# Kernel tuning notes

Hardware: AMD Instinct MI355X
Metric: run time of the kernel (lower is better)

The kernel has to match this reference:

```python
import jax, jax.numpy as jnp
import numpy as np

B, S, E, H = 4, 2048, 512, 8
DH = E // H
EPS = 1e-5

def _ln(x, g, b):
    m = jnp.mean(x, axis=-1, keepdims=True)
    v = jnp.var(x, axis=-1, keepdims=True)
    return (x - m) * jax.lax.rsqrt(v + EPS) * g + b

def setup_inputs() -> dict:
    key = jax.random.key(0)
    ks = jax.random.split(key, 8)
    sc = 0.02
    return {
        "x": jax.random.normal(ks[0], (B, S, E), dtype=jnp.float32),
        "ln1_g": jnp.ones((E,), jnp.float32),
        "ln1_b": jnp.zeros((E,), jnp.float32),
        "in_proj_w": sc * jax.random.normal(ks[1], (3 * E, E), jnp.float32),
        "in_proj_b": jnp.zeros((3 * E,), jnp.float32),
        "out_w": sc * jax.random.normal(ks[2], (E, E), jnp.float32),
        "out_b": jnp.zeros((E,), jnp.float32),
        "ln2_g": jnp.ones((E,), jnp.float32),
        "ln2_b": jnp.zeros((E,), jnp.float32),
        "fc1_w": sc * jax.random.normal(ks[3], (E, E), jnp.float32),
        "fc1_b": jnp.zeros((E,), jnp.float32),
        "fc2_w": sc * jax.random.normal(ks[4], (E, E), jnp.float32),
        "fc2_b": jnp.zeros((E,), jnp.float32),
    }

def reference(x, ln1_g, ln1_b, in_proj_w, in_proj_b, out_w, out_b,
              ln2_g, ln2_b, fc1_w, fc1_b, fc2_w, fc2_b):
    # pre-LN
    z = _ln(x, ln1_g, ln1_b)
    # qkv projection (torch MHA packed in_proj: [3E, E])
    qkv = z @ in_proj_w.T + in_proj_b          # [B,S,3E]
    q, k, v = jnp.split(qkv, 3, axis=-1)
    q = q.reshape(B, S, H, DH)
    k = k.reshape(B, S, H, DH)
    v = v.reshape(B, S, H, DH)
    scores = jnp.einsum("bqhd,bkhd->bhqk", q, k) / np.sqrt(DH).astype(np.float32)
    causal = jnp.triu(jnp.ones((S, S), dtype=bool), k=1)  # True = masked
    neg = jnp.finfo(scores.dtype).min
    scores = jnp.where(causal, neg, scores)
    attn = jax.nn.softmax(scores, axis=-1)      # [B,H,S,S]
    ctx = jnp.einsum("bhqk,bkhd->bqhd", attn, v).reshape(B, S, E)
    attn_out = ctx @ out_w.T + out_b
    # torch MHA with need_weights=True averages over heads by default
    attn_weights = jnp.mean(attn, axis=1)       # [B,S,S]
    z2 = x + attn_out
    y = _ln(z2, ln2_g, ln2_b)
    y = jax.nn.leaky_relu(y @ fc1_w.T + fc1_b, negative_slope=0.01)
    y = y @ fc2_w.T + fc2_b
    y = y + z2
    return (y, attn_weights)
```

## Files before the change

### kernel.cpp

```cpp
#include <hip/hip_runtime.h>

typedef short bf16x8 __attribute__((ext_vector_type(8)));
typedef float f32x4 __attribute__((ext_vector_type(4)));
typedef unsigned short u16x8 __attribute__((ext_vector_type(8)));

#define NB 4
#define SQ 2048
#define EM 512
#define NH 8
#define DHD 64
#define QSCALE 0.1803368801111731f

__device__ __forceinline__ unsigned short f2bf(float x) {
  unsigned u = __float_as_uint(x);
  u += 0x7FFFu + ((u >> 16) & 1u);
  return (unsigned short)(u >> 16);
}

__device__ __forceinline__ int sw8(int row, int col8) { return col8 ^ ((row & 7) << 3); }

__device__ __forceinline__ void glds16(const void* g, void* l) {
  __builtin_amdgcn_global_load_lds(
      (const __attribute__((address_space(1))) void*)g,
      (__attribute__((address_space(3))) void*)l, 16, 0, 0);
}

__global__ __launch_bounds__(256) void f2bf4_kernel(
    const float* __restrict__ w0, const float* __restrict__ w1,
    const float* __restrict__ w2, const float* __restrict__ w3,
    unsigned short* __restrict__ o0, unsigned short* __restrict__ o1,
    unsigned short* __restrict__ o2, unsigned short* __restrict__ o3) {
  int i = (blockIdx.x * 256 + threadIdx.x) * 8;
  const float* src;
  unsigned short* dst;
  int off;
  if (i < 786432) { src = w0; dst = o0; off = i; }
  else if (i < 1048576) { src = w1; dst = o1; off = i - 786432; }
  else if (i < 1310720) { src = w2; dst = o2; off = i - 1048576; }
  else { src = w3; dst = o3; off = i - 1310720; }
  f32x4 a = *(const f32x4*)(src + off);
  f32x4 b = *(const f32x4*)(src + off + 4);
  u16x8 o;
#pragma unroll
  for (int j = 0; j < 4; ++j) { o[j] = f2bf(a[j]); o[j + 4] = f2bf(b[j]); }
  *(u16x8*)(dst + off) = o;
}

__global__ __launch_bounds__(256) void ln_kernel(const float* __restrict__ x,
                                                 const float* __restrict__ g,
                                                 const float* __restrict__ bb,
                                                 unsigned short* __restrict__ out) {
  int tid = threadIdx.x;
  int row = blockIdx.x * 4 + (tid >> 6);
  int lane = tid & 63;
  size_t base = (size_t)row * EM + lane * 8;
  f32x4 v0 = *(const f32x4*)(x + base);
  f32x4 v1 = *(const f32x4*)(x + base + 4);
  float s = 0.f, q = 0.f;
#pragma unroll
  for (int j = 0; j < 4; ++j) { s += v0[j] + v1[j]; q += v0[j] * v0[j] + v1[j] * v1[j]; }
#pragma unroll
  for (int m = 1; m < 64; m <<= 1) { s += __shfl_xor(s, m); q += __shfl_xor(q, m); }
  float mean = s * (1.f / EM);
  float var = q * (1.f / EM) - mean * mean;
  float rs = rsqrtf(var + 1e-5f);
  f32x4 g0 = *(const f32x4*)(g + lane * 8), g1 = *(const f32x4*)(g + lane * 8 + 4);
  f32x4 b0 = *(const f32x4*)(bb + lane * 8), b1 = *(const f32x4*)(bb + lane * 8 + 4);
  u16x8 o;
#pragma unroll
  for (int j = 0; j < 4; ++j) {
    o[j] = f2bf((v0[j] - mean) * rs * g0[j] + b0[j]);
    o[j + 4] = f2bf((v1[j] - mean) * rs * g1[j] + b1[j]);
  }
  *(u16x8*)(out + base) = o;
}

template <bool LEAKY, bool RESID, bool OUTF32, bool QKV>
__global__ __launch_bounds__(256) void gemm64(
    const unsigned short* __restrict__ A, const unsigned short* __restrict__ Bm,
    const float* __restrict__ bias, const float* __restrict__ resid,
    float* __restrict__ outf, unsigned short* __restrict__ outh,
    unsigned short* __restrict__ qo, unsigned short* __restrict__ ko,
    unsigned short* __restrict__ vo, int M, int N, int K) {
  __shared__ unsigned short As[2][64][64];
  __shared__ unsigned short Bs[2][64][64];
  int m0 = blockIdx.x * 64, n0 = blockIdx.y * 64;
  int t = threadIdx.x;
  int wv = t >> 6, ln = t & 63, lg = ln >> 4, lr = ln & 15;
  int rsub = ln >> 3;
  int csw = ((ln & 7) ^ rsub) * 8;
  f32x4 acc[4];
#pragma unroll
  for (int c = 0; c < 4; ++c)
#pragma unroll
    for (int r = 0; r < 4; ++r) acc[c][r] = 0.f;

  const unsigned short* ag0 = A + (size_t)(m0 + wv * 16 + rsub) * K + csw;
  const unsigned short* ag1 = A + (size_t)(m0 + wv * 16 + 8 + rsub) * K + csw;
  const unsigned short* bg0 = Bm + (size_t)(n0 + wv * 16 + rsub) * K + csw;
  const unsigned short* bg1 = Bm + (size_t)(n0 + wv * 16 + 8 + rsub) * K + csw;

  glds16(ag0, &As[0][wv * 16][0]);
  glds16(ag1, &As[0][wv * 16 + 8][0]);
  glds16(bg0, &Bs[0][wv * 16][0]);
  glds16(bg1, &Bs[0][wv * 16 + 8][0]);

  int nk = K >> 6;
  for (int ki = 0; ki < nk; ++ki) {
    int cur = ki & 1;
    __syncthreads();
    if (ki + 1 < nk) {
      int nb = cur ^ 1;
      int ko_ = (ki + 1) * 64;
      glds16(ag0 + ko_, &As[nb][wv * 16][0]);
      glds16(ag1 + ko_, &As[nb][wv * 16 + 8][0]);
      glds16(bg0 + ko_, &Bs[nb][wv * 16][0]);
      glds16(bg1 + ko_, &Bs[nb][wv * 16 + 8][0]);
    }
#pragma unroll
    for (int kk = 0; kk < 64; kk += 32) {
      int arw = wv * 16 + lr;
      bf16x8 af = *(const bf16x8*)&As[cur][arw][sw8(arw, kk + lg * 8)];
#pragma unroll
      for (int c = 0; c < 4; ++c) {
        int brw = c * 16 + lr;
        bf16x8 bf = *(const bf16x8*)&Bs[cur][brw][sw8(brw, kk + lg * 8)];
        acc[c] = __builtin_amdgcn_mfma_f32_16x16x32_bf16(af, bf, acc[c], 0, 0, 0);
      }
    }
  }
#pragma unroll
  for (int c = 0; c < 4; ++c) {
    int C_ = n0 + c * 16 + lr;
    float bv = bias[C_];
#pragma unroll
    for (int r = 0; r < 4; ++r) {
      int R_ = m0 + wv * 16 + lg * 4 + r;
      float v = acc[c][r] + bv;
      if (LEAKY) v = v > 0.f ? v : 0.01f * v;
      if (RESID) v += resid[(size_t)R_ * N + C_];
      if (QKV) {
        int which = C_ >> 9, f = C_ & 511, h = f >> 6, d = f & 63;
        int b_ = R_ >> 11, s_ = R_ & 2047;
        if (which == 0) {
          qo[(((size_t)b_ * NH + h) * SQ + s_) * DHD + d] = f2bf(v * QSCALE);
        } else if (which == 1) {
          ko[(((size_t)b_ * NH + h) * SQ + s_) * DHD + d] = f2bf(v);
        } else {
          vo[(((size_t)b_ * NH + h) * DHD + d) * SQ + s_] = f2bf(v);
        }
      } else if (OUTF32) {
        outf[(size_t)R_ * N + C_] = v;
      } else {
        outh[(size_t)R_ * N + C_] = f2bf(v);
      }
    }
  }
}

template <bool QKV>
__global__ __launch_bounds__(256) void gemm128(
    const unsigned short* __restrict__ A, const unsigned short* __restrict__ Bm,
    const float* __restrict__ bias, unsigned short* __restrict__ qo,
    unsigned short* __restrict__ ko, unsigned short* __restrict__ vo,
    int M, int N, int K) {
  __shared__ unsigned short As[2][128][64];
  __shared__ unsigned short Bs[2][128][64];
  int m0 = blockIdx.x * 128, n0 = blockIdx.y * 128;
  int t = threadIdx.x;
  int wv = t >> 6, ln = t & 63, lg = ln >> 4, lr = ln & 15;
  int wr = wv >> 1, wc = wv & 1;
  int rsub = ln >> 3;
  int csw = ((ln & 7) ^ rsub) * 8;
  f32x4 acc[4][4];
#pragma unroll
  for (int m = 0; m < 4; ++m)
#pragma unroll
    for (int n = 0; n < 4; ++n)
#pragma unroll
      for (int r = 0; r < 4; ++r) acc[m][n][r] = 0.f;

  const unsigned short* agb = A + (size_t)(m0 + wv * 8 + rsub) * K + csw;
  const unsigned short* bgb = Bm + (size_t)(n0 + wv * 8 + rsub) * K + csw;

#pragma unroll
  for (int i = 0; i < 4; ++i) {
    glds16(agb + (size_t)(i * 32) * K, &As[0][i * 32 + wv * 8][0]);
    glds16(bgb + (size_t)(i * 32) * K, &Bs[0][i * 32 + wv * 8][0]);
  }

  int nk = K >> 6;
  for (int ki = 0; ki < nk; ++ki) {
    int cur = ki & 1;
    __syncthreads();
    if (ki + 1 < nk) {
      int nb = cur ^ 1;
      int ko_ = (ki + 1) * 64;
#pragma unroll
      for (int i = 0; i < 4; ++i) {
        glds16(agb + (size_t)(i * 32) * K + ko_, &As[nb][i * 32 + wv * 8][0]);
        glds16(bgb + (size_t)(i * 32) * K + ko_, &Bs[nb][i * 32 + wv * 8][0]);
      }
    }
#pragma unroll
    for (int kk = 0; kk < 64; kk += 32) {
      bf16x8 af[4], bfr[4];
#pragma unroll
      for (int m = 0; m < 4; ++m) {
        int arw = wr * 64 + m * 16 + lr;
        af[m] = *(const bf16x8*)&As[cur][arw][sw8(arw, kk + lg * 8)];
      }
#pragma unroll
      for (int n = 0; n < 4; ++n) {
        int brw = wc * 64 + n * 16 + lr;
        bfr[n] = *(const bf16x8*)&Bs[cur][brw][sw8(brw, kk + lg * 8)];
      }
#pragma unroll
      for (int m = 0; m < 4; ++m)
#pragma unroll
        for (int n = 0; n < 4; ++n)
          acc[m][n] = __builtin_amdgcn_mfma_f32_16x16x32_bf16(af[m], bfr[n], acc[m][n], 0, 0, 0);
    }
  }

#pragma unroll
  for (int n = 0; n < 4; ++n) {
    int C_ = n0 + wc * 64 + n * 16 + lr;
    float bv = bias[C_];
#pragma unroll
    for (int m = 0; m < 4; ++m) {
#pragma unroll
      for (int r = 0; r < 4; ++r) {
        int R_ = m0 + wr * 64 + m * 16 + lg * 4 + r;
        float v = acc[m][n][r] + bv;
        int which = C_ >> 9, f = C_ & 511, h = f >> 6, d = f & 63;
        int b_ = R_ >> 11, s_ = R_ & 2047;
        if (which == 0) {
          qo[(((size_t)b_ * NH + h) * SQ + s_) * DHD + d] = f2bf(v * QSCALE);
        } else if (which == 1) {
          ko[(((size_t)b_ * NH + h) * SQ + s_) * DHD + d] = f2bf(v);
        } else {
          vo[(((size_t)b_ * NH + h) * DHD + d) * SQ + s_] = f2bf(v);
        }
      }
    }
  }
}

__global__ __launch_bounds__(256) void flash_kernel(
    const unsigned short* __restrict__ Q, const unsigned short* __restrict__ Kb,
    const unsigned short* __restrict__ Vt, unsigned short* __restrict__ ctx,
    float* __restrict__ mstat, float* __restrict__ lstat) {
  __shared__ unsigned short Ks[2][64][64];
  __shared__ unsigned short Vs[2][64][64];
  __shared__ unsigned short Ps[4][16][64];
  int h = blockIdx.y, b = blockIdx.z;
  int t = threadIdx.x, wv = t >> 6, ln = t & 63, lg = ln >> 4, lr = ln & 15;
  int rsub = ln >> 3;
  int csw = ((ln & 7) ^ rsub) * 8;
  size_t headoff = ((size_t)b * NH + h) * SQ;
  const unsigned short* kg0 = Kb + (headoff + wv * 16 + rsub) * DHD + csw;
  const unsigned short* kg1 = Kb + (headoff + wv * 16 + 8 + rsub) * DHD + csw;
  const unsigned short* vg0 = Vt + (((size_t)b * NH + h) * DHD + wv * 16 + rsub) * SQ + csw;
  const unsigned short* vg1 = Vt + (((size_t)b * NH + h) * DHD + wv * 16 + 8 + rsub) * SQ + csw;

  bf16x8 vones;
#pragma unroll
  for (int j = 0; j < 8; ++j) vones[j] = (lr == 0) ? (short)0x3F80 : (short)0;

  for (int half = 0; half < 2; ++half) {
    int qt = half ? blockIdx.x : (31 - blockIdx.x);
    int qb = qt * 64;
    const unsigned short* qrow = Q + (headoff + qb + wv * 16 + lr) * DHD;
    bf16x8 aq0 = *(const bf16x8*)(qrow + lg * 8);
    bf16x8 aq1 = *(const bf16x8*)(qrow + 32 + lg * 8);

    f32x4 cacc[4], lacc;
#pragma unroll
    for (int nd = 0; nd < 4; ++nd)
#pragma unroll
      for (int r = 0; r < 4; ++r) cacc[nd][r] = 0.f;
#pragma unroll
    for (int r = 0; r < 4; ++r) lacc[r] = 0.f;
    float mrun[4];
#pragma unroll
    for (int r = 0; r < 4; ++r) mrun[r] = -__builtin_inff();

    int nkt = qt + 1;
    __syncthreads();
    glds16(kg0, &Ks[0][wv * 16][0]);
    glds16(kg1, &Ks[0][wv * 16 + 8][0]);
    glds16(vg0, &Vs[0][wv * 16][0]);
    glds16(vg1, &Vs[0][wv * 16 + 8][0]);

    for (int kt = 0; kt < nkt; ++kt) {
      int cur = kt & 1;
      __syncthreads();
      if (kt + 1 < nkt) {
        int nb = cur ^ 1;
        size_t ko_ = (size_t)(kt + 1) * 64;
        glds16(kg0 + ko_ * DHD, &Ks[nb][wv * 16][0]);
        glds16(kg1 + ko_ * DHD, &Ks[nb][wv * 16 + 8][0]);
        glds16(vg0 + ko_, &Vs[nb][wv * 16][0]);
        glds16(vg1 + ko_, &Vs[nb][wv * 16 + 8][0]);
      }

      float sv[4][4];
      __builtin_amdgcn_s_setprio(1);
#pragma unroll
      for (int nt = 0; nt < 4; ++nt) {
        f32x4 sf;
#pragma unroll
        for (int r = 0; r < 4; ++r) sf[r] = 0.f;
        int brw = nt * 16 + lr;
        bf16x8 bk0 = *(const bf16x8*)&Ks[cur][brw][sw8(brw, lg * 8)];
        bf16x8 bk1 = *(const bf16x8*)&Ks[cur][brw][sw8(brw, 32 + lg * 8)];
        sf = __builtin_amdgcn_mfma_f32_16x16x32_bf16(aq0, bk0, sf, 0, 0, 0);
        sf = __builtin_amdgcn_mfma_f32_16x16x32_bf16(aq1, bk1, sf, 0, 0, 0);
#pragma unroll
        for (int r = 0; r < 4; ++r) sv[nt][r] = sf[r];
      }
      __builtin_amdgcn_s_setprio(0);
      if (kt == nkt - 1) {
        int kbase = kt * 64;
#pragma unroll
        for (int nt = 0; nt < 4; ++nt) {
          int kcol = kbase + nt * 16 + lr;
#pragma unroll
          for (int r = 0; r < 4; ++r) {
            int qr = qb + wv * 16 + lg * 4 + r;
            if (kcol > qr) sv[nt][r] = -__builtin_inff();
          }
        }
      }

      float lmax[4];
      bool need = false;
#pragma unroll
      for (int r = 0; r < 4; ++r) {
        lmax[r] = fmaxf(fmaxf(sv[0][r], sv[1][r]), fmaxf(sv[2][r], sv[3][r]));
        need |= (lmax[r] > mrun[r] + 8.f);
      }
      if (__any(need)) {
#pragma unroll
        for (int r = 0; r < 4; ++r) {
          float tm = lmax[r];
#pragma unroll
          for (int m = 1; m < 16; m <<= 1) tm = fmaxf(tm, __shfl_xor(tm, m));
          float mn = fmaxf(mrun[r], tm);
          float sc = exp2f(mrun[r] - mn);
          mrun[r] = mn;
          lacc[r] *= sc;
#pragma unroll
          for (int nd = 0; nd < 4; ++nd) cacc[nd][r] *= sc;
        }
      }
#pragma unroll
      for (int r = 0; r < 4; ++r) {
        int prow = lg * 4 + r;
#pragma unroll
        for (int nt = 0; nt < 4; ++nt) {
          float p = exp2f(sv[nt][r] - mrun[r]);
          Ps[wv][prow][sw8(prow, nt * 16 + lr)] = f2bf(p);
        }
      }

      bf16x8 pf0 = *(const bf16x8*)&Ps[wv][lr][sw8(lr, lg * 8)];
      bf16x8 pf1 = *(const bf16x8*)&Ps[wv][lr][sw8(lr, 32 + lg * 8)];
      __builtin_amdgcn_s_setprio(1);
      lacc = __builtin_amdgcn_mfma_f32_16x16x32_bf16(pf0, vones, lacc, 0, 0, 0);
      lacc = __builtin_amdgcn_mfma_f32_16x16x32_bf16(pf1, vones, lacc, 0, 0, 0);
#pragma unroll
      for (int nd = 0; nd < 4; ++nd) {
        int vrw = nd * 16 + lr;
        bf16x8 vf0 = *(const bf16x8*)&Vs[cur][vrw][sw8(vrw, lg * 8)];
        bf16x8 vf1 = *(const bf16x8*)&Vs[cur][vrw][sw8(vrw, 32 + lg * 8)];
        cacc[nd] = __builtin_amdgcn_mfma_f32_16x16x32_bf16(pf0, vf0, cacc[nd], 0, 0, 0);
        cacc[nd] = __builtin_amdgcn_mfma_f32_16x16x32_bf16(pf1, vf1, cacc[nd], 0, 0, 0);
      }
      __builtin_amdgcn_s_setprio(0);
    }

    float inv[4];
#pragma unroll
    for (int r = 0; r < 4; ++r) inv[r] = 1.f / __shfl(lacc[r], ln & 48);
#pragma unroll
    for (int nd = 0; nd < 4; ++nd)
#pragma unroll
      for (int r = 0; r < 4; ++r) {
        size_t dst = ((size_t)b * SQ + qb + wv * 16 + lg * 4 + r) * EM + h * DHD + nd * 16 + lr;
        ctx[dst] = f2bf(cacc[nd][r] * inv[r]);
      }
    if (lr == 0) {
#pragma unroll
      for (int r = 0; r < 4; ++r) {
        int row = qb + wv * 16 + lg * 4 + r;
        mstat[headoff + row] = mrun[r];
        lstat[headoff + row] = 0.125f * inv[r];
      }
    }
  }
}

__global__ __launch_bounds__(256) void attnw_kernel(
    const unsigned short* __restrict__ Q, const unsigned short* __restrict__ Kb,
    const float* __restrict__ mstat, const float* __restrict__ lstat,
    float* __restrict__ aw) {
  int kt = blockIdx.x, qt = blockIdx.y, b = blockIdx.z;
  int qb = qt * 64, kb = kt * 64;
  int t = threadIdx.x;
  float* tile = aw + ((size_t)b * SQ + qb) * SQ + kb;
  if (kt > qt) {
    int row = t >> 2, c = (t & 3) * 16;
    f32x4 z;
#pragma unroll
    for (int j = 0; j < 4; ++j) z[j] = 0.f;
    float* p = tile + (size_t)row * SQ + c;
    *(f32x4*)p = z; *(f32x4*)(p + 4) = z; *(f32x4*)(p + 8) = z; *(f32x4*)(p + 12) = z;
    return;
  }
  __shared__ unsigned short Ks[2][64][64];
  int wv = t >> 6, ln = t & 63, lg = ln >> 4, lr = ln & 15;
  int rsub = ln >> 3;
  int csw = ((ln & 7) ^ rsub) * 8;
  bool diag = (kt == qt);
  size_t khstride = (size_t)SQ * DHD;
  const unsigned short* kg0 = Kb + (((size_t)b * NH) * SQ + kb + wv * 16 + rsub) * DHD + csw;
  const unsigned short* kg1 = Kb + (((size_t)b * NH) * SQ + kb + wv * 16 + 8 + rsub) * DHD + csw;
  const unsigned short* qg = Q + (((size_t)b * NH) * SQ + qb + wv * 16 + lr) * DHD + lg * 8;
  size_t mbase = (size_t)b * NH * SQ + qb + wv * 16 + lg * 4;

  glds16(kg0, &Ks[0][wv * 16][0]);
  glds16(kg1, &Ks[0][wv * 16 + 8][0]);

  bf16x8 aqc0 = *(const bf16x8*)qg;
  bf16x8 aqc1 = *(const bf16x8*)(qg + 32);
  bf16x8 aqn0 = *(const bf16x8*)(qg + khstride);
  bf16x8 aqn1 = *(const bf16x8*)(qg + khstride + 32);
  float mmc[4], lic[4], mmn[4], lin[4];
#pragma unroll
  for (int r = 0; r < 4; ++r) {
    mmc[r] = mstat[mbase + r];
    lic[r] = lstat[mbase + r];
    mmn[r] = mstat[mbase + SQ + r];
    lin[r] = lstat[mbase + SQ + r];
  }

  f32x4 facc[4];
#pragma unroll
  for (int nt = 0; nt < 4; ++nt)
#pragma unroll
    for (int r = 0; r < 4; ++r) facc[nt][r] = 0.f;

  for (int h = 0; h < NH; ++h) {
    int cur = h & 1;
    __syncthreads();
    if (h + 1 < NH) {
      glds16(kg0 + (size_t)(h + 1) * khstride, &Ks[cur ^ 1][wv * 16][0]);
      glds16(kg1 + (size_t)(h + 1) * khstride, &Ks[cur ^ 1][wv * 16 + 8][0]);
    }

#pragma unroll
    for (int nt = 0; nt < 4; ++nt) {
      f32x4 sf;
#pragma unroll
      for (int r = 0; r < 4; ++r) sf[r] = 0.f;
      int brw = nt * 16 + lr;
      bf16x8 bk0 = *(const bf16x8*)&Ks[cur][brw][sw8(brw, lg * 8)];
      bf16x8 bk1 = *(const bf16x8*)&Ks[cur][brw][sw8(brw, 32 + lg * 8)];
      sf = __builtin_amdgcn_mfma_f32_16x16x32_bf16(aqc0, bk0, sf, 0, 0, 0);
      sf = __builtin_amdgcn_mfma_f32_16x16x32_bf16(aqc1, bk1, sf, 0, 0, 0);
#pragma unroll
      for (int r = 0; r < 4; ++r) facc[nt][r] += exp2f(sf[r] - mmc[r]) * lic[r];
    }

    aqc0 = aqn0; aqc1 = aqn1;
#pragma unroll
    for (int r = 0; r < 4; ++r) { mmc[r] = mmn[r]; lic[r] = lin[r]; }
    if (h + 2 < NH) {
      aqn0 = *(const bf16x8*)(qg + (size_t)(h + 2) * khstride);
      aqn1 = *(const bf16x8*)(qg + (size_t)(h + 2) * khstride + 32);
#pragma unroll
      for (int r = 0; r < 4; ++r) {
        mmn[r] = mstat[mbase + (size_t)(h + 2) * SQ + r];
        lin[r] = lstat[mbase + (size_t)(h + 2) * SQ + r];
      }
    }
  }

#pragma unroll
  for (int nt = 0; nt < 4; ++nt) {
    int kc = kb + nt * 16 + lr;
#pragma unroll
    for (int r = 0; r < 4; ++r) {
      int qr = qb + wv * 16 + lg * 4 + r;
      float v = (diag && kc > qr) ? 0.f : facc[nt][r];
      tile[(size_t)(wv * 16 + lg * 4 + r) * SQ + nt * 16 + lr] = v;
    }
  }
}

extern "C" void kernel_launch(void* const* d_in, const int* in_sizes, int n_in,
                              void* d_out, int out_size, void* d_ws, size_t ws_size,
                              hipStream_t stream) {
  (void)in_sizes; (void)n_in; (void)out_size; (void)ws_size;
  const float* x = (const float*)d_in[0];
  const float* ln1g = (const float*)d_in[1];
  const float* ln1b = (const float*)d_in[2];
  const float* wqkv = (const float*)d_in[3];
  const float* bqkv = (const float*)d_in[4];
  const float* wout = (const float*)d_in[5];
  const float* bout = (const float*)d_in[6];
  const float* ln2g = (const float*)d_in[7];
  const float* ln2b = (const float*)d_in[8];
  const float* wfc1 = (const float*)d_in[9];
  const float* bfc1 = (const float*)d_in[10];
  const float* wfc2 = (const float*)d_in[11];
  const float* bfc2 = (const float*)d_in[12];

  char* ws = (char*)d_ws;
  unsigned short* zctx = (unsigned short*)(ws);
  unsigned short* qb_ = (unsigned short*)(ws + 8388608);
  unsigned short* kb_ = (unsigned short*)(ws + 16777216);
  unsigned short* vb_ = (unsigned short*)(ws + 25165824);
  float* z2 = (float*)(ws + 33554432);
  float* mstat = (float*)(ws + 50331648);
  float* lstat = (float*)(ws + 50593792);
  unsigned short* wqkv_h = (unsigned short*)(ws + 50855936);
  unsigned short* wout_h = (unsigned short*)(ws + 52428800);
  unsigned short* wfc1_h = (unsigned short*)(ws + 52953088);
  unsigned short* wfc2_h = (unsigned short*)(ws + 53477376);
  unsigned short* y1 = qb_;
  unsigned short* h1 = kb_;

  float* outy = (float*)d_out;
  float* outw = outy + (size_t)NB * SQ * EM;

  f2bf4_kernel<<<768, 256, 0, stream>>>(wqkv, wout, wfc1, wfc2,
                                        wqkv_h, wout_h, wfc1_h, wfc2_h);

  ln_kernel<<<2048, 256, 0, stream>>>(x, ln1g, ln1b, zctx);
  gemm128<true><<<dim3(64, 12), 256, 0, stream>>>(
      zctx, wqkv_h, bqkv, qb_, kb_, vb_, 8192, 1536, 512);
  flash_kernel<<<dim3(16, 8, 4), 256, 0, stream>>>(qb_, kb_, vb_, zctx, mstat, lstat);
  attnw_kernel<<<dim3(32, 32, 4), 256, 0, stream>>>(qb_, kb_, mstat, lstat, outw);
  gemm64<false, true, true, false><<<dim3(128, 8), 256, 0, stream>>>(
      zctx, wout_h, bout, x, z2, nullptr, nullptr, nullptr, nullptr, 8192, 512, 512);
  ln_kernel<<<2048, 256, 0, stream>>>(z2, ln2g, ln2b, y1);
  gemm64<true, false, false, false><<<dim3(128, 8), 256, 0, stream>>>(
      y1, wfc1_h, bfc1, nullptr, nullptr, h1, nullptr, nullptr, nullptr, 8192, 512, 512);
  gemm64<false, true, true, false><<<dim3(128, 8), 256, 0, stream>>>(
      h1, wfc2_h, bfc2, z2, outy, nullptr, nullptr, nullptr, nullptr, 8192, 512, 512);
}
```

Baseline: 192.8 us.

## Use 512-thread flash blocks with 128-row query tiles sharing K/V loads

The flash attention kernel now runs 8 waves per block over a single 128-row query tile, instead of 4 waves each processing two paired 64-row tiles in sequence. Each K/V tile loaded into LDS is therefore reused by twice as many query rows, and each wave loads half as much K/V. Load balance comes from interleaving tile indices across blocks instead of pairing tiles inside a block. In exchange, waves with lower query rows compute an extra masked diagonal tile, and register and LDS pressure per block rise.

```diff
diff --git a/kernel.cpp b/kernel.cpp
--- a/kernel.cpp
+++ b/kernel.cpp
@@ -247,157 +247,150 @@
   }
 }
 
-__global__ __launch_bounds__(256) void flash_kernel(
+__global__ __launch_bounds__(512) void flash_kernel(
     const unsigned short* __restrict__ Q, const unsigned short* __restrict__ Kb,
     const unsigned short* __restrict__ Vt, unsigned short* __restrict__ ctx,
     float* __restrict__ mstat, float* __restrict__ lstat) {
   __shared__ unsigned short Ks[2][64][64];
   __shared__ unsigned short Vs[2][64][64];
-  __shared__ unsigned short Ps[4][16][64];
-  int h = blockIdx.y, b = blockIdx.z;
+  __shared__ unsigned short Ps[8][16][64];
+  int bx = blockIdx.x, h = blockIdx.y, b = blockIdx.z;
+  int i2 = bx >> 1;
+  int j = (bx & 1) ? i2 : (15 - i2);
+  int qb = j * 128;
   int t = threadIdx.x, wv = t >> 6, ln = t & 63, lg = ln >> 4, lr = ln & 15;
   int rsub = ln >> 3;
   int csw = ((ln & 7) ^ rsub) * 8;
+  int qrow0 = qb + wv * 16;
   size_t headoff = ((size_t)b * NH + h) * SQ;
-  const unsigned short* kg0 = Kb + (headoff + wv * 16 + rsub) * DHD + csw;
-  const unsigned short* kg1 = Kb + (headoff + wv * 16 + 8 + rsub) * DHD + csw;
-  const unsigned short* vg0 = Vt + (((size_t)b * NH + h) * DHD + wv * 16 + rsub) * SQ + csw;
-  const unsigned short* vg1 = Vt + (((size_t)b * NH + h) * DHD + wv * 16 + 8 + rsub) * SQ + csw;
+  const unsigned short* kg = Kb + (headoff + wv * 8 + rsub) * DHD + csw;
+  const unsigned short* vg = Vt + (((size_t)b * NH + h) * DHD + wv * 8 + rsub) * SQ + csw;
+
+  const unsigned short* qrow = Q + (headoff + qrow0 + lr) * DHD;
+  bf16x8 aq0 = *(const bf16x8*)(qrow + lg * 8);
+  bf16x8 aq1 = *(const bf16x8*)(qrow + 32 + lg * 8);
 
   bf16x8 vones;
 #pragma unroll
-  for (int j = 0; j < 8; ++j) vones[j] = (lr == 0) ? (short)0x3F80 : (short)0;
-
-  for (int half = 0; half < 2; ++half) {
-    int qt = half ? blockIdx.x : (31 - blockIdx.x);
-    int qb = qt * 64;
-    const unsigned short* qrow = Q + (headoff + qb + wv * 16 + lr) * DHD;
-    bf16x8 aq0 = *(const bf16x8*)(qrow + lg * 8);
-    bf16x8 aq1 = *(const bf16x8*)(qrow + 32 + lg * 8);
-
-    f32x4 cacc[4], lacc;
-#pragma unroll
-    for (int nd = 0; nd < 4; ++nd)
-#pragma unroll
-      for (int r = 0; r < 4; ++r) cacc[nd][r] = 0.f;
-#pragma unroll
-    for (int r = 0; r < 4; ++r) lacc[r] = 0.f;
-    float mrun[4];
-#pragma unroll
-    for (int r = 0; r < 4; ++r) mrun[r] = -__builtin_inff();
-
-    int nkt = qt + 1;
+  for (int jj = 0; jj < 8; ++jj) vones[jj] = (lr == 0) ? (short)0x3F80 : (short)0;
+
+  f32x4 cacc[4], lacc;
+#pragma unroll
+  for (int nd = 0; nd < 4; ++nd)
+#pragma unroll
+    for (int r = 0; r < 4; ++r) cacc[nd][r] = 0.f;
+#pragma unroll
+  for (int r = 0; r < 4; ++r) lacc[r] = 0.f;
+  float mrun[4];
+#pragma unroll
+  for (int r = 0; r < 4; ++r) mrun[r] = -__builtin_inff();
+
+  int nkt = (qb >> 6) + 2;
+  glds16(kg, &Ks[0][wv * 8][0]);
+  glds16(vg, &Vs[0][wv * 8][0]);
+
+  for (int kt = 0; kt < nkt; ++kt) {
+    int cur = kt & 1;
     __syncthreads();
-    glds16(kg0, &Ks[0][wv * 16][0]);
-    glds16(kg1, &Ks[0][wv * 16 + 8][0]);
-    glds16(vg0, &Vs[0][wv * 16][0]);
-    glds16(vg1, &Vs[0][wv * 16 + 8][0]);
-
-    for (int kt = 0; kt < nkt; ++kt) {
-      int cur = kt & 1;
-      __syncthreads();
-      if (kt + 1 < nkt) {
-        int nb = cur ^ 1;
-        size_t ko_ = (size_t)(kt + 1) * 64;
-        glds16(kg0 + ko_ * DHD, &Ks[nb][wv * 16][0]);
-        glds16(kg1 + ko_ * DHD, &Ks[nb][wv * 16 + 8][0]);
-        glds16(vg0 + ko_, &Vs[nb][wv * 16][0]);
-        glds16(vg1 + ko_, &Vs[nb][wv * 16 + 8][0]);
-      }
-
-      float sv[4][4];
-      __builtin_amdgcn_s_setprio(1);
+    if (kt + 1 < nkt) {
+      int nb = cur ^ 1;
+      size_t ko_ = (size_t)(kt + 1) * 64;
+      glds16(kg + ko_ * DHD, &Ks[nb][wv * 8][0]);
+      glds16(vg + ko_, &Vs[nb][wv * 8][0]);
+    }
+
+    float sv[4][4];
+    __builtin_amdgcn_s_setprio(1);
+#pragma unroll
+    for (int nt = 0; nt < 4; ++nt) {
+      f32x4 sf;
+#pragma unroll
+      for (int r = 0; r < 4; ++r) sf[r] = 0.f;
+      int brw = nt * 16 + lr;
+      bf16x8 bk0 = *(const bf16x8*)&Ks[cur][brw][sw8(brw, lg * 8)];
+      bf16x8 bk1 = *(const bf16x8*)&Ks[cur][brw][sw8(brw, 32 + lg * 8)];
+      sf = __builtin_amdgcn_mfma_f32_16x16x32_bf16(aq0, bk0, sf, 0, 0, 0);
+      sf = __builtin_amdgcn_mfma_f32_16x16x32_bf16(aq1, bk1, sf, 0, 0, 0);
+#pragma unroll
+      for (int r = 0; r < 4; ++r) sv[nt][r] = sf[r];
+    }
+    __builtin_amdgcn_s_setprio(0);
+    if (kt * 64 + 63 > qrow0) {
+      int kbase = kt * 64;
 #pragma unroll
       for (int nt = 0; nt < 4; ++nt) {
-        f32x4 sf;
-#pragma unroll
-        for (int r = 0; r < 4; ++r) sf[r] = 0.f;
-        int brw = nt * 16 + lr;
-        bf16x8 bk0 = *(const bf16x8*)&Ks[cur][brw][sw8(brw, lg * 8)];
-        bf16x8 bk1 = *(const bf16x8*)&Ks[cur][brw][sw8(brw, 32 + lg * 8)];
-        sf = __builtin_amdgcn_mfma_f32_16x16x32_bf16(aq0, bk0, sf, 0, 0, 0);
-        sf = __builtin_amdgcn_mfma_f32_16x16x32_bf16(aq1, bk1, sf, 0, 0, 0);
-#pragma unroll
-        for (int r = 0; r < 4; ++r) sv[nt][r] = sf[r];
-      }
-      __builtin_amdgcn_s_setprio(0);
-      if (kt == nkt - 1) {
-        int kbase = kt * 64;
-#pragma unroll
-        for (int nt = 0; nt < 4; ++nt) {
-          int kcol = kbase + nt * 16 + lr;
-#pragma unroll
-          for (int r = 0; r < 4; ++r) {
-            int qr = qb + wv * 16 + lg * 4 + r;
-            if (kcol > qr) sv[nt][r] = -__builtin_inff();
-          }
+        int kcol = kbase + nt * 16 + lr;
+#pragma unroll
+        for (int r = 0; r < 4; ++r) {
+          int qr = qrow0 + lg * 4 + r;
+          if (kcol > qr) sv[nt][r] = -__builtin_inff();
         }
       }
-
-      float lmax[4];
-      bool need = false;
+    }
+
+    float lmax[4];
+    bool need = false;
+#pragma unroll
+    for (int r = 0; r < 4; ++r) {
+      lmax[r] = fmaxf(fmaxf(sv[0][r], sv[1][r]), fmaxf(sv[2][r], sv[3][r]));
+      need |= (lmax[r] > mrun[r] + 8.f);
+    }
+    if (__any(need)) {
 #pragma unroll
       for (int r = 0; r < 4; ++r) {
-        lmax[r] = fmaxf(fmaxf(sv[0][r], sv[1][r]), fmaxf(sv[2][r], sv[3][r]));
-        need |= (lmax[r] > mrun[r] + 8.f);
-      }
-      if (__any(need)) {
-#pragma unroll
-        for (int r = 0; r < 4; ++r) {
-          float tm = lmax[r];
-#pragma unroll
-          for (int m = 1; m < 16; m <<= 1) tm = fmaxf(tm, __shfl_xor(tm, m));
-          float mn = fmaxf(mrun[r], tm);
-          float sc = exp2f(mrun[r] - mn);
-          mrun[r] = mn;
-          lacc[r] *= sc;
-#pragma unroll
-          for (int nd = 0; nd < 4; ++nd) cacc[nd][r] *= sc;
-        }
-      }
-#pragma unroll
-      for (int r = 0; r < 4; ++r) {
-        int prow = lg * 4 + r;
-#pragma unroll
-        for (int nt = 0; nt < 4; ++nt) {
-          float p = exp2f(sv[nt][r] - mrun[r]);
-          Ps[wv][prow][sw8(prow, nt * 16 + lr)] = f2bf(p);
-        }
-      }
-
-      bf16x8 pf0 = *(const bf16x8*)&Ps[wv][lr][sw8(lr, lg * 8)];
-      bf16x8 pf1 = *(const bf16x8*)&Ps[wv][lr][sw8(lr, 32 + lg * 8)];
-      __builtin_amdgcn_s_setprio(1);
-      lacc = __builtin_amdgcn_mfma_f32_16x16x32_bf16(pf0, vones, lacc, 0, 0, 0);
-      lacc = __builtin_amdgcn_mfma_f32_16x16x32_bf16(pf1, vones, lacc, 0, 0, 0);
-#pragma unroll
-      for (int nd = 0; nd < 4; ++nd) {
-        int vrw = nd * 16 + lr;
-        bf16x8 vf0 = *(const bf16x8*)&Vs[cur][vrw][sw8(vrw, lg * 8)];
-        bf16x8 vf1 = *(const bf16x8*)&Vs[cur][vrw][sw8(vrw, 32 + lg * 8)];
-        cacc[nd] = __builtin_amdgcn_mfma_f32_16x16x32_bf16(pf0, vf0, cacc[nd], 0, 0, 0);
-        cacc[nd] = __builtin_amdgcn_mfma_f32_16x16x32_bf16(pf1, vf1, cacc[nd], 0, 0, 0);
-      }
-      __builtin_amdgcn_s_setprio(0);
-    }
-
-    float inv[4];
-#pragma unroll
-    for (int r = 0; r < 4; ++r) inv[r] = 1.f / __shfl(lacc[r], ln & 48);
-#pragma unroll
-    for (int nd = 0; nd < 4; ++nd)
-#pragma unroll
-      for (int r = 0; r < 4; ++r) {
-        size_t dst = ((size_t)b * SQ + qb + wv * 16 + lg * 4 + r) * EM + h * DHD + nd * 16 + lr;
-        ctx[dst] = f2bf(cacc[nd][r] * inv[r]);
-      }
-    if (lr == 0) {
-#pragma unroll
-      for (int r = 0; r < 4; ++r) {
-        int row = qb + wv * 16 + lg * 4 + r;
-        mstat[headoff + row] = mrun[r];
-        lstat[headoff + row] = 0.125f * inv[r];
-      }
+        float tm = lmax[r];
+#pragma unroll
+        for (int m = 1; m < 16; m <<= 1) tm = fmaxf(tm, __shfl_xor(tm, m));
+        float mn = fmaxf(mrun[r], tm);
+        float sc = exp2f(mrun[r] - mn);
+        mrun[r] = mn;
+        lacc[r] *= sc;
+#pragma unroll
+        for (int nd = 0; nd < 4; ++nd) cacc[nd][r] *= sc;
+      }
+    }
+#pragma unroll
+    for (int r = 0; r < 4; ++r) {
+      int prow = lg * 4 + r;
+#pragma unroll
+      for (int nt = 0; nt < 4; ++nt) {
+        float p = exp2f(sv[nt][r] - mrun[r]);
+        Ps[wv][prow][sw8(prow, nt * 16 + lr)] = f2bf(p);
+      }
+    }
+
+    bf16x8 pf0 = *(const bf16x8*)&Ps[wv][lr][sw8(lr, lg * 8)];
+    bf16x8 pf1 = *(const bf16x8*)&Ps[wv][lr][sw8(lr, 32 + lg * 8)];
+    __builtin_amdgcn_s_setprio(1);
+    lacc = __builtin_amdgcn_mfma_f32_16x16x32_bf16(pf0, vones, lacc, 0, 0, 0);
+    lacc = __builtin_amdgcn_mfma_f32_16x16x32_bf16(pf1, vones, lacc, 0, 0, 0);
+#pragma unroll
+    for (int nd = 0; nd < 4; ++nd) {
+      int vrw = nd * 16 + lr;
+      bf16x8 vf0 = *(const bf16x8*)&Vs[cur][vrw][sw8(vrw, lg * 8)];
+      bf16x8 vf1 = *(const bf16x8*)&Vs[cur][vrw][sw8(vrw, 32 + lg * 8)];
+      cacc[nd] = __builtin_amdgcn_mfma_f32_16x16x32_bf16(pf0, vf0, cacc[nd], 0, 0, 0);
+      cacc[nd] = __builtin_amdgcn_mfma_f32_16x16x32_bf16(pf1, vf1, cacc[nd], 0, 0, 0);
+    }
+    __builtin_amdgcn_s_setprio(0);
+  }
+
+  float inv[4];
+#pragma unroll
+  for (int r = 0; r < 4; ++r) inv[r] = 1.f / __shfl(lacc[r], ln & 48);
+#pragma unroll
+  for (int nd = 0; nd < 4; ++nd)
+#pragma unroll
+    for (int r = 0; r < 4; ++r) {
+      size_t dst = ((size_t)b * SQ + qrow0 + lg * 4 + r) * EM + h * DHD + nd * 16 + lr;
+      ctx[dst] = f2bf(cacc[nd][r] * inv[r]);
+    }
+  if (lr == 0) {
+#pragma unroll
+    for (int r = 0; r < 4; ++r) {
+      int row = qrow0 + lg * 4 + r;
+      mstat[headoff + row] = mrun[r];
+      lstat[headoff + row] = 0.125f * inv[r];
     }
   }
 }
@@ -542,7 +535,7 @@
   ln_kernel<<<2048, 256, 0, stream>>>(x, ln1g, ln1b, zctx);
   gemm128<true><<<dim3(64, 12), 256, 0, stream>>>(
       zctx, wqkv_h, bqkv, qb_, kb_, vb_, 8192, 1536, 512);
-  flash_kernel<<<dim3(16, 8, 4), 256, 0, stream>>>(qb_, kb_, vb_, zctx, mstat, lstat);
+  flash_kernel<<<dim3(16, 8, 4), 512, 0, stream>>>(qb_, kb_, vb_, zctx, mstat, lstat);
   attnw_kernel<<<dim3(32, 32, 4), 256, 0, stream>>>(qb_, kb_, mstat, lstat, outw);
   gemm64<false, true, true, false><<<dim3(128, 8), 256, 0, stream>>>(
       zctx, wout_h, bout, x, z2, nullptr, nullptr, nullptr, nullptr, 8192, 512, 512);
```

After: 209.9 us. 1.09x slower.
